# Kernel tuning notes

Hardware: AMD Instinct MI355X
Metric: run time of the kernel (lower is better)

Reference implementation:

```python
import jax, jax.numpy as jnp
import numpy as np

B, C, T = 128, 64, 128   # batch, num_channels (EEG electrodes), EEG_SEGMENT_LENGTH
HID = 128                # hidden_dim
E = HID // 2             # attention embed dim = 64
NH = 4                   # attention heads


def setup_inputs() -> dict:
    key = jax.random.key(0)
    ks = jax.random.split(key, 12)
    s = lambda k, shp, sc: jax.random.normal(k, shp, dtype=jnp.float32) * sc
    return {
        "eeg_data": jax.random.normal(ks[0], (B, C, T), dtype=jnp.float32),
        "gcn1_w": s(ks[1], (HID, T), 0.05),   # nn.Linear(T, HID): W [out,in]
        "gcn1_b": jnp.zeros((HID,), jnp.float32),
        "gcn2_w": s(ks[2], (E, HID), 0.05),
        "gcn2_b": jnp.zeros((E,), jnp.float32),
        "bn1_g": jnp.ones((C,), jnp.float32),
        "bn1_b": jnp.zeros((C,), jnp.float32),
        "bn2_g": jnp.ones((C,), jnp.float32),
        "bn2_b": jnp.zeros((C,), jnp.float32),
        "attn_in_w": s(ks[3], (3 * E, E), 0.08),   # packed q,k,v projection
        "attn_in_b": jnp.zeros((3 * E,), jnp.float32),
        "attn_out_w": s(ks[4], (E, E), 0.08),
        "attn_out_b": jnp.zeros((E,), jnp.float32),
    }


def _hilbert_phase(x):
    # torch.fft.fft -> zero bins [n//2:] (even n) -> *2 -> ifft -> angle
    n = x.shape[-1]
    half = n // 2 if n % 2 == 0 else (n + 1) // 2
    X = jnp.fft.fft(x, axis=-1)
    mask = (jnp.arange(n) < half).astype(jnp.float32) * 2.0
    analytic = jnp.fft.ifft(X * mask, axis=-1)
    return jnp.angle(analytic)


def _wpli(eeg):
    phase = _hilbert_phase(eeg)                         # [B,C,T]
    pd = phase[:, :, None, :] - phase[:, None, :, :]    # [B,C,C,T]
    pli = jnp.abs(jnp.mean(jnp.sign(jnp.sin(pd)), axis=-1))  # [B,C,C]
    eye = jnp.eye(pli.shape[-1], dtype=pli.dtype)
    return pli * (1.0 - eye)[None]


def _gcn(x, adj, w, b):
    # D^{-1/2} A D^{-1/2} via row/col scaling (equiv to diag_embed + bmm)
    deg = jnp.sum(adj, axis=2)                          # [B,C]
    dn = 1.0 / jnp.sqrt(deg + 1e-8)
    adj_n = adj * dn[:, :, None] * dn[:, None, :]
    support = jnp.einsum('bij,bjf->bif', adj_n, x)
    return support @ w.T + b


def _bn(x, g, b):
    # BatchNorm1d over channel dim C of [B,C,F]; batch stats over (B,F)
    m = jnp.mean(x, axis=(0, 2), keepdims=True)
    v = jnp.var(x, axis=(0, 2), keepdims=True)
    return (x - m) / jnp.sqrt(v + 1e-5) * g[None, :, None] + b[None, :, None]


def _mha(x, in_w, in_b, out_w, out_b):
    bsz, n, e = x.shape
    hd = e // NH
    qkv = x @ in_w.T + in_b                             # [B,N,3E]
    q, k, v = jnp.split(qkv, 3, axis=-1)
    sp = lambda t: t.reshape(bsz, n, NH, hd).transpose(0, 2, 1, 3)  # [B,H,N,hd]
    q, k, v = sp(q), sp(k), sp(v)
    scores = jnp.einsum('bhqd,bhkd->bhqk', q, k) / jnp.sqrt(jnp.float32(hd))
    attn = jax.nn.softmax(scores, axis=-1)
    o = jnp.einsum('bhqk,bhkd->bhqd', attn, v)
    o = o.transpose(0, 2, 1, 3).reshape(bsz, n, e)
    return o @ out_w.T + out_b


def reference(eeg_data, gcn1_w, gcn1_b, gcn2_w, gcn2_b, bn1_g, bn1_b,
              bn2_g, bn2_b, attn_in_w, attn_in_b, attn_out_w, attn_out_b):
    wpli = _wpli(eeg_data)                              # [B,C,C]
    x = jax.nn.relu(_bn(_gcn(eeg_data, wpli, gcn1_w, gcn1_b), bn1_g, bn1_b))
    x = jax.nn.relu(_bn(_gcn(x, wpli, gcn2_w, gcn2_b), bn2_g, bn2_b))
    x = _mha(x, attn_in_w, attn_in_b, attn_out_w, attn_out_b)
    features = jnp.mean(x, axis=1)                      # [B, E]
    return features, wpli
```

## Files before the change

### kernel.cpp

```cpp
#include <hip/hip_runtime.h>
#include <math.h>

#define NB 128
#define NC 64
#define NT 128
#define HIDN 128
#define NE 64
#define NHD 4
#define HD 16

__global__ void analytic_kernel(const float* __restrict__ eeg,
                                float* __restrict__ re, float* __restrict__ im) {
    int row = blockIdx.x;
    int t = threadIdx.x;
    __shared__ float xs[NT];
    __shared__ double cotv[64];
    xs[t] = eeg[row * NT + t];
    if (t < 64) {
        double d = (double)(2 * t + 1);
        double a = 3.14159265358979323846 * d / 128.0;
        cotv[t] = cos(a) / sin(a);
    }
    __syncthreads();
    double ar = 0.0, ai = 0.0;
    #pragma unroll
    for (int m = 0; m < 64; ++m) {
        int d = 2 * m + 1;
        int s = (t - d) & 127;
        double xv = (double)xs[s];
        ar += xv;
        ai += cotv[m] * xv;
    }
    double rr = (double)xs[t] + ar * (1.0 / 64.0);
    double ii = ai * (1.0 / 64.0);
    re[row * NT + t] = (float)rr;
    im[row * NT + t] = (float)ii;
}

__global__ void pli_kernel(const float* __restrict__ re, const float* __restrict__ im,
                           float* __restrict__ wpli, float* __restrict__ deg) {
    int b = blockIdx.x >> 4;
    int i0 = (blockIdx.x & 15) << 2;
    int tid = threadIdx.x;
    int w = tid >> 6;
    int j = tid & 63;
    __shared__ float4 sre4[64 * 32];
    __shared__ float4 sim4[64 * 32];
    __shared__ int pacc[4][4][64];
    const float* reb = re + b * (NC * NT);
    const float* imb = im + b * (NC * NT);
    for (int idx4 = tid; idx4 < 2048; idx4 += 256) {
        int c = idx4 >> 5, t4 = idx4 & 31;
        int slot = c * 32 + (t4 ^ (c & 31));
        sre4[slot] = ((const float4*)reb)[idx4];
        sim4[slot] = ((const float4*)imb)[idx4];
    }
    __syncthreads();
    int acc0 = 0, acc1 = 0, acc2 = 0, acc3 = 0;
    #pragma unroll
    for (int tt = 0; tt < 8; ++tt) {
        int t4 = w * 8 + tt;
        float4 rj = sre4[j * 32 + (t4 ^ (j & 31))];
        float4 ij = sim4[j * 32 + (t4 ^ (j & 31))];
        #pragma unroll
        for (int di = 0; di < 4; ++di) {
            int i = i0 + di;
            float4 ri = sre4[i * 32 + (t4 ^ (i & 31))];
            float4 ii = sim4[i * 32 + (t4 ^ (i & 31))];
            float c0 = ii.x * rj.x - ri.x * ij.x;
            float c1 = ii.y * rj.y - ri.y * ij.y;
            float c2 = ii.z * rj.z - ri.z * ij.z;
            float c3 = ii.w * rj.w - ri.w * ij.w;
            int d = ((c0 > 0.f) ? 1 : ((c0 < 0.f) ? -1 : 0))
                  + ((c1 > 0.f) ? 1 : ((c1 < 0.f) ? -1 : 0))
                  + ((c2 > 0.f) ? 1 : ((c2 < 0.f) ? -1 : 0))
                  + ((c3 > 0.f) ? 1 : ((c3 < 0.f) ? -1 : 0));
            if (di == 0) acc0 += d;
            else if (di == 1) acc1 += d;
            else if (di == 2) acc2 += d;
            else acc3 += d;
        }
    }
    pacc[w][0][j] = acc0; pacc[w][1][j] = acc1;
    pacc[w][2][j] = acc2; pacc[w][3][j] = acc3;
    __syncthreads();
    int di2 = tid >> 6, j2 = tid & 63;
    int a = pacc[0][di2][j2] + pacc[1][di2][j2] + pacc[2][di2][j2] + pacc[3][di2][j2];
    float p = fabsf((float)a * (1.f / (float)NT));
    int i = i0 + di2;
    if (j2 == i) p = 0.f;
    wpli[b * (NC * NC) + i * NC + j2] = p;
    float s = p;
    #pragma unroll
    for (int off = 32; off > 0; off >>= 1) s += __shfl_down(s, off);
    if (j2 == 0) deg[b * NC + i] = s;
}

template <int OUT, bool BN_IN>
__global__ __launch_bounds__(1024, 1) void gcn_fused(
        const float* __restrict__ adj, const float* __restrict__ deg,
        const float* __restrict__ x, const double* __restrict__ dpart_in,
        const float* __restrict__ g, const float* __restrict__ bb,
        const float* __restrict__ W, const float* __restrict__ bias,
        float* __restrict__ xout, double* __restrict__ dpart_out) {
    int b = blockIdx.x >> 1;
    int half = blockIdx.x & 1;
    int tid = threadIdx.x;
    __shared__ float dn_s[64];
    __shared__ float stat_s[64][2];
    __shared__ float arow[32][68];
    __shared__ float xs[64][128];
    __shared__ float sup[32][132];
    __shared__ float WsT[128][(OUT == 128) ? 132 : 68];
    __shared__ double dred[16][64][2];

    if (BN_IN) {
        int c = tid & 63, chunk = tid >> 6;
        double s = 0.0, s2 = 0.0;
        for (int bi = chunk * 8; bi < chunk * 8 + 8; ++bi) {
            s  += dpart_in[(bi * 64 + c) * 2];
            s2 += dpart_in[(bi * 64 + c) * 2 + 1];
        }
        dred[chunk][c][0] = s;
        dred[chunk][c][1] = s2;
    }
    if (tid < 64)
        dn_s[tid] = (float)(1.0 / sqrt((double)deg[b * 64 + tid] + 1e-8));
    __syncthreads();
    if (BN_IN && tid < 64) {
        double s = 0.0, s2 = 0.0;
        for (int ch = 0; ch < 16; ++ch) {
            s  += dred[ch][tid][0];
            s2 += dred[ch][tid][1];
        }
        double N = (double)(NB * HIDN);
        double m = s / N;
        double var = s2 / N - m * m;
        stat_s[tid][0] = (float)m;
        stat_s[tid][1] = (float)(1.0 / sqrt(var + 1e-5));
    }
    __syncthreads();
    if (tid < 512) {
        int il = tid >> 4, j4 = tid & 15;
        int i = half * 32 + il;
        float4 v = *(const float4*)&adj[b * 4096 + i * 64 + j4 * 4];
        float di = dn_s[i];
        v.x *= di * dn_s[j4 * 4 + 0];
        v.y *= di * dn_s[j4 * 4 + 1];
        v.z *= di * dn_s[j4 * 4 + 2];
        v.w *= di * dn_s[j4 * 4 + 3];
        *(float4*)&arow[il][j4 * 4] = v;
    }
    #pragma unroll
    for (int p = 0; p < 2; ++p) {
        int idx4 = tid + p * 1024;
        int r = idx4 >> 5, c4 = idx4 & 31;
        float4 v = ((const float4*)(x + b * 8192))[idx4];
        if (BN_IN) {
            float m = stat_s[r][0], rs = stat_s[r][1], gg = g[r], bv = bb[r];
            v.x = (v.x - m) * rs * gg + bv; v.x = v.x > 0.f ? v.x : 0.f;
            v.y = (v.y - m) * rs * gg + bv; v.y = v.y > 0.f ? v.y : 0.f;
            v.z = (v.z - m) * rs * gg + bv; v.z = v.z > 0.f ? v.z : 0.f;
            v.w = (v.w - m) * rs * gg + bv; v.w = v.w > 0.f ? v.w : 0.f;
        }
        *(float4*)&xs[r][c4 * 4] = v;
    }
    #pragma unroll
    for (int p = 0; p < OUT / 32; ++p) {
        int idx4 = tid + p * 1024;
        int o = idx4 & (OUT - 1);
        int k4 = idx4 / OUT;
        float4 w = *(const float4*)&W[o * 128 + k4 * 4];
        WsT[k4 * 4 + 0][o] = w.x;
        WsT[k4 * 4 + 1][o] = w.y;
        WsT[k4 * 4 + 2][o] = w.z;
        WsT[k4 * 4 + 3][o] = w.w;
    }
    __syncthreads();

    int il = tid >> 5;
    int i = half * 32 + il;
    {
        int f0 = (tid & 31) * 4;
        float a0 = 0.f, a1 = 0.f, a2 = 0.f, a3 = 0.f;
        #pragma unroll 8
        for (int j = 0; j < 64; ++j) {
            float a = arow[il][j];
            float4 xv = *(const float4*)&xs[j][f0];
            a0 += a * xv.x; a1 += a * xv.y; a2 += a * xv.z; a3 += a * xv.w;
        }
        *(float4*)&sup[il][f0] = make_float4(a0, a1, a2, a3);
    }
    __syncthreads();

    double ds = 0.0, ds2 = 0.0;
    if (OUT == 128) {
        int o0 = (tid & 31) * 4;
        float c[4] = {};
        #pragma unroll 8
        for (int k = 0; k < 128; ++k) {
            float s = sup[il][k];
            float4 w0 = *(const float4*)&WsT[k][o0];
            c[0] += s * w0.x; c[1] += s * w0.y; c[2] += s * w0.z; c[3] += s * w0.w;
        }
        float4 r0 = make_float4(c[0] + bias[o0], c[1] + bias[o0 + 1],
                                c[2] + bias[o0 + 2], c[3] + bias[o0 + 3]);
        *(float4*)&xout[b * 64 * 128 + i * 128 + o0] = r0;
        ds  = (double)r0.x + (double)r0.y + (double)r0.z + (double)r0.w;
        ds2 = (double)r0.x * r0.x + (double)r0.y * r0.y
            + (double)r0.z * r0.z + (double)r0.w * r0.w;
    } else {
        int o0 = (tid & 31) * 2;
        float c0 = 0.f, c1 = 0.f;
        #pragma unroll 8
        for (int k = 0; k < 128; ++k) {
            float s = sup[il][k];
            c0 += s * WsT[k][o0];
            c1 += s * WsT[k][o0 + 1];
        }
        c0 += bias[o0];
        c1 += bias[o0 + 1];
        *(float2*)&xout[b * 64 * 64 + i * 64 + o0] = make_float2(c0, c1);
        ds  = (double)c0 + (double)c1;
        ds2 = (double)c0 * c0 + (double)c1 * c1;
    }
    #pragma unroll
    for (int off = 16; off > 0; off >>= 1) {
        ds  += __shfl_down(ds, off, 32);
        ds2 += __shfl_down(ds2, off, 32);
    }
    if ((tid & 31) == 0) {
        dpart_out[(b * 64 + i) * 2]     = ds;
        dpart_out[(b * 64 + i) * 2 + 1] = ds2;
    }
}

__global__ __launch_bounds__(1024, 1) void attn_fused(
        const float* __restrict__ x2, const double* __restrict__ dpart2,
        const float* __restrict__ g, const float* __restrict__ bb,
        const float* __restrict__ Win, const float* __restrict__ bin,
        const float* __restrict__ Wout, const float* __restrict__ bout,
        float* __restrict__ feat) {
    int b = blockIdx.x;
    int tid = threadIdx.x;
    int lane = tid & 63, wv = tid >> 6;
    __shared__ float stat_s[64][2];
    __shared__ float xs[64][68];
    __shared__ float ws[192][64];
    __shared__ float kqkv[192][64];
    __shared__ float pm_s[4][256], ps_s[4][256];
    __shared__ float pool_s[64][17];
    __shared__ float mo[64];

    if (tid < 64) {
        double s = 0.0, s2 = 0.0;
        for (int bi = 0; bi < NB; ++bi) {
            s  += dpart2[(bi * 64 + tid) * 2];
            s2 += dpart2[(bi * 64 + tid) * 2 + 1];
        }
        double N = (double)(NB * NE);
        double m = s / N;
        double var = s2 / N - m * m;
        stat_s[tid][0] = (float)m;
        stat_s[tid][1] = (float)(1.0 / sqrt(var + 1e-5));
    }
    #pragma unroll
    for (int p = 0; p < 3; ++p) {
        int idx4 = tid + p * 1024;
        int o = idx4 >> 4, c4 = idx4 & 15;
        *(float4*)&ws[o][c4 * 4] = ((const float4*)(Win + o * 64))[c4];
    }
    __syncthreads();
    {
        int r = tid >> 4, c4 = tid & 15;
        float4 v = ((const float4*)(x2 + b * 4096))[tid];
        float m = stat_s[r][0], rs = stat_s[r][1], gg = g[r], bv = bb[r];
        v.x = (v.x - m) * rs * gg + bv; v.x = v.x > 0.f ? v.x : 0.f;
        v.y = (v.y - m) * rs * gg + bv; v.y = v.y > 0.f ? v.y : 0.f;
        v.z = (v.z - m) * rs * gg + bv; v.z = v.z > 0.f ? v.z : 0.f;
        v.w = (v.w - m) * rs * gg + bv; v.w = v.w > 0.f ? v.w : 0.f;
        *(float4*)&xs[r][c4 * 4] = v;
    }
    __syncthreads();

    float xr[64];
    #pragma unroll
    for (int d4 = 0; d4 < 16; ++d4) {
        float4 v = *(const float4*)&xs[lane][d4 * 4];
        xr[d4 * 4 + 0] = v.x; xr[d4 * 4 + 1] = v.y;
        xr[d4 * 4 + 2] = v.z; xr[d4 * 4 + 3] = v.w;
    }
    float acc[12];
    #pragma unroll
    for (int u = 0; u < 12; ++u) acc[u] = bin[wv + 16 * u];
    #pragma unroll
    for (int d4 = 0; d4 < 16; ++d4) {
        #pragma unroll
        for (int u = 0; u < 12; ++u) {
            float4 w = *(const float4*)&ws[wv + 16 * u][d4 * 4];
            acc[u] += xr[d4 * 4 + 0] * w.x + xr[d4 * 4 + 1] * w.y
                    + xr[d4 * 4 + 2] * w.z + xr[d4 * 4 + 3] * w.w;
        }
    }
    #pragma unroll
    for (int u = 0; u < 12; ++u) kqkv[wv + 16 * u][lane] = acc[u];
    __syncthreads();

    int h = wv >> 2, jc = wv & 3;
    int e0 = 16 * h, j0 = jc * 16, hn = h * 64 + lane;
    float q[16];
    #pragma unroll
    for (int d = 0; d < 16; ++d) q[d] = kqkv[e0 + d][lane];
    float sc[16];
    #pragma unroll
    for (int jj = 0; jj < 16; ++jj) sc[jj] = 0.f;
    #pragma unroll
    for (int d = 0; d < 16; ++d) {
        float qd = q[d];
        #pragma unroll
        for (int j4 = 0; j4 < 4; ++j4) {
            float4 kv = *(const float4*)&kqkv[64 + e0 + d][j0 + j4 * 4];
            sc[j4 * 4 + 0] += qd * kv.x;
            sc[j4 * 4 + 1] += qd * kv.y;
            sc[j4 * 4 + 2] += qd * kv.z;
            sc[j4 * 4 + 3] += qd * kv.w;
        }
    }
    float pmax = -1e30f;
    #pragma unroll
    for (int jj = 0; jj < 16; ++jj) { sc[jj] *= 0.25f; pmax = fmaxf(pmax, sc[jj]); }
    pm_s[jc][hn] = pmax;
    __syncthreads();
    float mx = fmaxf(fmaxf(pm_s[0][hn], pm_s[1][hn]),
                     fmaxf(pm_s[2][hn], pm_s[3][hn]));
    float psum = 0.f;
    #pragma unroll
    for (int jj = 0; jj < 16; ++jj) { sc[jj] = expf(sc[jj] - mx); psum += sc[jj]; }
    ps_s[jc][hn] = psum;
    float po[16];
    #pragma unroll
    for (int d = 0; d < 16; ++d) {
        float4 v0 = *(const float4*)&kqkv[128 + e0 + d][j0 + 0];
        float4 v1 = *(const float4*)&kqkv[128 + e0 + d][j0 + 4];
        float4 v2 = *(const float4*)&kqkv[128 + e0 + d][j0 + 8];
        float4 v3 = *(const float4*)&kqkv[128 + e0 + d][j0 + 12];
        po[d] = sc[0] * v0.x + sc[1] * v0.y + sc[2] * v0.z + sc[3] * v0.w
              + sc[4] * v1.x + sc[5] * v1.y + sc[6] * v1.z + sc[7] * v1.w
              + sc[8] * v2.x + sc[9] * v2.y + sc[10] * v2.z + sc[11] * v2.w
              + sc[12] * v3.x + sc[13] * v3.y + sc[14] * v3.z + sc[15] * v3.w;
    }
    __syncthreads();
    float inv = 1.f / (ps_s[0][hn] + ps_s[1][hn] + ps_s[2][hn] + ps_s[3][hn]);
    if (jc == 0) {
        #pragma unroll
        for (int d = 0; d < 16; ++d) kqkv[e0 + d][lane] = po[d];
    }
    __syncthreads();
    if (jc == 1) {
        #pragma unroll
        for (int d = 0; d < 16; ++d) kqkv[e0 + d][lane] += po[d];
    }
    __syncthreads();
    if (jc == 2) {
        #pragma unroll
        for (int d = 0; d < 16; ++d) kqkv[e0 + d][lane] += po[d];
    }
    __syncthreads();
    if (jc == 3) {
        #pragma unroll
        for (int d = 0; d < 16; ++d)
            kqkv[e0 + d][lane] = (kqkv[e0 + d][lane] + po[d]) * inv;
    }
    __syncthreads();
    {
        int e = tid >> 4, part = tid & 15;
        float4 v = *(const float4*)&kqkv[e][part * 4];
        pool_s[e][part] = v.x + v.y + v.z + v.w;
    }
    __syncthreads();
    if (tid < 64) {
        float s = 0.f;
        #pragma unroll
        for (int p = 0; p < 16; ++p) s += pool_s[tid][p];
        mo[tid] = s * (1.f / 64.f);
    }
    __syncthreads();
    if (tid < 64) {
        float a = bout[tid];
        const float4* wr = (const float4*)(Wout + tid * 64);
        #pragma unroll
        for (int d4 = 0; d4 < 16; ++d4) {
            float4 w = wr[d4];
            a += mo[d4 * 4 + 0] * w.x + mo[d4 * 4 + 1] * w.y
               + mo[d4 * 4 + 2] * w.z + mo[d4 * 4 + 3] * w.w;
        }
        feat[b * NE + tid] = a;
    }
}

extern "C" void kernel_launch(void* const* d_in, const int* in_sizes, int n_in,
                              void* d_out, int out_size, void* d_ws, size_t ws_size,
                              hipStream_t stream) {
    const float* eeg      = (const float*)d_in[0];
    const float* gcn1_w   = (const float*)d_in[1];
    const float* gcn1_b   = (const float*)d_in[2];
    const float* gcn2_w   = (const float*)d_in[3];
    const float* gcn2_b   = (const float*)d_in[4];
    const float* bn1_g    = (const float*)d_in[5];
    const float* bn1_b    = (const float*)d_in[6];
    const float* bn2_g    = (const float*)d_in[7];
    const float* bn2_b    = (const float*)d_in[8];
    const float* attn_in_w  = (const float*)d_in[9];
    const float* attn_in_b  = (const float*)d_in[10];
    const float* attn_out_w = (const float*)d_in[11];
    const float* attn_out_b = (const float*)d_in[12];

    float* out  = (float*)d_out;
    float* feat = out;
    float* wpli = out + NB * NE;

    float* ws = (float*)d_ws;
    float*  w_re   = ws;
    float*  w_im   = ws + 1048576;
    float*  w_x1   = ws + 2097152;
    float*  w_x2   = ws + 3145728;
    float*  w_deg  = ws + 3670016;
    double* dpart1 = (double*)(ws + 3678208);
    double* dpart2 = (double*)(ws + 3710976);

    analytic_kernel<<<NB * NC, NT, 0, stream>>>(eeg, w_re, w_im);
    pli_kernel<<<NB * NC / 4, 256, 0, stream>>>(w_re, w_im, wpli, w_deg);
    gcn_fused<HIDN, false><<<NB * 2, 1024, 0, stream>>>(
        wpli, w_deg, eeg, nullptr, nullptr, nullptr,
        gcn1_w, gcn1_b, w_x1, dpart1);
    gcn_fused<NE, true><<<NB * 2, 1024, 0, stream>>>(
        wpli, w_deg, w_x1, dpart1, bn1_g, bn1_b,
        gcn2_w, gcn2_b, w_x2, dpart2);
    attn_fused<<<NB, 1024, 0, stream>>>(w_x2, dpart2, bn2_g, bn2_b,
                                        attn_in_w, attn_in_b,
                                        attn_out_w, attn_out_b, feat);
}
```

Baseline: 103.2 us.

## Split attention kernel per head and move output projection to separate kernel

Replaces the one-block-per-batch 1024-thread attention kernel with 512 blocks of 256 threads, each handling one (batch, head) pair and loading only that head's slice of the QKV weights. The BN2 statistics reduction is spread across four waves instead of a single wave, and the pooled per-head outputs are written to workspace for a new small kernel that applies the output projection. The aim is more blocks and smaller shared-memory footprints so more CUs are busy, at the cost of an extra launch, a global round trip, and every block redundantly reducing the BN stats and normalizing the whole 64x64 input.

```diff
diff --git a/kernel.cpp b/kernel.cpp
--- a/kernel.cpp
+++ b/kernel.cpp
@@ -235,45 +235,45 @@
     }
 }
 
-__global__ __launch_bounds__(1024, 1) void attn_fused(
+__global__ __launch_bounds__(256) void attn_head(
         const float* __restrict__ x2, const double* __restrict__ dpart2,
         const float* __restrict__ g, const float* __restrict__ bb,
         const float* __restrict__ Win, const float* __restrict__ bin,
-        const float* __restrict__ Wout, const float* __restrict__ bout,
-        float* __restrict__ feat) {
-    int b = blockIdx.x;
+        float* __restrict__ w_mo) {
+    int b = blockIdx.x >> 2, h = blockIdx.x & 3;
     int tid = threadIdx.x;
     int lane = tid & 63, wv = tid >> 6;
+    __shared__ double dred[4][64][2];
     __shared__ float stat_s[64][2];
     __shared__ float xs[64][68];
-    __shared__ float ws[192][64];
-    __shared__ float kqkv[192][64];
-    __shared__ float pm_s[4][256], ps_s[4][256];
-    __shared__ float pool_s[64][17];
-    __shared__ float mo[64];
-
+    __shared__ float ws[48][64];
+    __shared__ float kqkv[48][64];
+    __shared__ float pm_s[4][64], ps_s[4][64];
+    __shared__ float pool_s[16][17];
+
+    {
+        double s = 0.0, s2 = 0.0;
+        for (int bi = wv * 32; bi < wv * 32 + 32; ++bi) {
+            s  += dpart2[(bi * 64 + lane) * 2];
+            s2 += dpart2[(bi * 64 + lane) * 2 + 1];
+        }
+        dred[wv][lane][0] = s;
+        dred[wv][lane][1] = s2;
+    }
+    __syncthreads();
     if (tid < 64) {
-        double s = 0.0, s2 = 0.0;
-        for (int bi = 0; bi < NB; ++bi) {
-            s  += dpart2[(bi * 64 + tid) * 2];
-            s2 += dpart2[(bi * 64 + tid) * 2 + 1];
-        }
+        double s  = dred[0][tid][0] + dred[1][tid][0] + dred[2][tid][0] + dred[3][tid][0];
+        double s2 = dred[0][tid][1] + dred[1][tid][1] + dred[2][tid][1] + dred[3][tid][1];
         double N = (double)(NB * NE);
         double m = s / N;
         double var = s2 / N - m * m;
         stat_s[tid][0] = (float)m;
         stat_s[tid][1] = (float)(1.0 / sqrt(var + 1e-5));
     }
-    #pragma unroll
-    for (int p = 0; p < 3; ++p) {
-        int idx4 = tid + p * 1024;
-        int o = idx4 >> 4, c4 = idx4 & 15;
-        *(float4*)&ws[o][c4 * 4] = ((const float4*)(Win + o * 64))[c4];
-    }
-    __syncthreads();
-    {
-        int r = tid >> 4, c4 = tid & 15;
-        float4 v = ((const float4*)(x2 + b * 4096))[tid];
+    __syncthreads();
+    for (int idx4 = tid; idx4 < 1024; idx4 += 256) {
+        int r = idx4 >> 4, c4 = idx4 & 15;
+        float4 v = ((const float4*)(x2 + b * 4096))[idx4];
         float m = stat_s[r][0], rs = stat_s[r][1], gg = g[r], bv = bb[r];
         v.x = (v.x - m) * rs * gg + bv; v.x = v.x > 0.f ? v.x : 0.f;
         v.y = (v.y - m) * rs * gg + bv; v.y = v.y > 0.f ? v.y : 0.f;
@@ -281,36 +281,36 @@
         v.w = (v.w - m) * rs * gg + bv; v.w = v.w > 0.f ? v.w : 0.f;
         *(float4*)&xs[r][c4 * 4] = v;
     }
-    __syncthreads();
-
-    float xr[64];
+    for (int idx4 = tid; idx4 < 768; idx4 += 256) {
+        int rl = idx4 >> 4, c4 = idx4 & 15;
+        int rg = ((rl >> 4) << 6) + (h << 4) + (rl & 15);
+        *(float4*)&ws[rl][c4 * 4] = ((const float4*)(Win + rg * 64))[c4];
+    }
+    __syncthreads();
+
+    float acc[12];
+    #pragma unroll
+    for (int u = 0; u < 12; ++u) {
+        int ol = wv + 4 * u;
+        acc[u] = bin[((ol >> 4) << 6) + (h << 4) + (ol & 15)];
+    }
     #pragma unroll
     for (int d4 = 0; d4 < 16; ++d4) {
-        float4 v = *(const float4*)&xs[lane][d4 * 4];
-        xr[d4 * 4 + 0] = v.x; xr[d4 * 4 + 1] = v.y;
-        xr[d4 * 4 + 2] = v.z; xr[d4 * 4 + 3] = v.w;
-    }
-    float acc[12];
-    #pragma unroll
-    for (int u = 0; u < 12; ++u) acc[u] = bin[wv + 16 * u];
-    #pragma unroll
-    for (int d4 = 0; d4 < 16; ++d4) {
+        float4 xv = *(const float4*)&xs[lane][d4 * 4];
         #pragma unroll
         for (int u = 0; u < 12; ++u) {
-            float4 w = *(const float4*)&ws[wv + 16 * u][d4 * 4];
-            acc[u] += xr[d4 * 4 + 0] * w.x + xr[d4 * 4 + 1] * w.y
-                    + xr[d4 * 4 + 2] * w.z + xr[d4 * 4 + 3] * w.w;
-        }
-    }
-    #pragma unroll
-    for (int u = 0; u < 12; ++u) kqkv[wv + 16 * u][lane] = acc[u];
-    __syncthreads();
-
-    int h = wv >> 2, jc = wv & 3;
-    int e0 = 16 * h, j0 = jc * 16, hn = h * 64 + lane;
+            float4 w = *(const float4*)&ws[wv + 4 * u][d4 * 4];
+            acc[u] += xv.x * w.x + xv.y * w.y + xv.z * w.z + xv.w * w.w;
+        }
+    }
+    #pragma unroll
+    for (int u = 0; u < 12; ++u) kqkv[wv + 4 * u][lane] = acc[u];
+    __syncthreads();
+
+    int j0 = wv * 16;
     float q[16];
     #pragma unroll
-    for (int d = 0; d < 16; ++d) q[d] = kqkv[e0 + d][lane];
+    for (int d = 0; d < 16; ++d) q[d] = kqkv[d][lane];
     float sc[16];
     #pragma unroll
     for (int jj = 0; jj < 16; ++jj) sc[jj] = 0.f;
@@ -319,7 +319,7 @@
         float qd = q[d];
         #pragma unroll
         for (int j4 = 0; j4 < 4; ++j4) {
-            float4 kv = *(const float4*)&kqkv[64 + e0 + d][j0 + j4 * 4];
+            float4 kv = *(const float4*)&kqkv[16 + d][j0 + j4 * 4];
             sc[j4 * 4 + 0] += qd * kv.x;
             sc[j4 * 4 + 1] += qd * kv.y;
             sc[j4 * 4 + 2] += qd * kv.z;
@@ -329,73 +329,81 @@
     float pmax = -1e30f;
     #pragma unroll
     for (int jj = 0; jj < 16; ++jj) { sc[jj] *= 0.25f; pmax = fmaxf(pmax, sc[jj]); }
-    pm_s[jc][hn] = pmax;
-    __syncthreads();
-    float mx = fmaxf(fmaxf(pm_s[0][hn], pm_s[1][hn]),
-                     fmaxf(pm_s[2][hn], pm_s[3][hn]));
+    pm_s[wv][lane] = pmax;
+    __syncthreads();
+    float mx = fmaxf(fmaxf(pm_s[0][lane], pm_s[1][lane]),
+                     fmaxf(pm_s[2][lane], pm_s[3][lane]));
     float psum = 0.f;
     #pragma unroll
     for (int jj = 0; jj < 16; ++jj) { sc[jj] = expf(sc[jj] - mx); psum += sc[jj]; }
-    ps_s[jc][hn] = psum;
+    ps_s[wv][lane] = psum;
     float po[16];
     #pragma unroll
     for (int d = 0; d < 16; ++d) {
-        float4 v0 = *(const float4*)&kqkv[128 + e0 + d][j0 + 0];
-        float4 v1 = *(const float4*)&kqkv[128 + e0 + d][j0 + 4];
-        float4 v2 = *(const float4*)&kqkv[128 + e0 + d][j0 + 8];
-        float4 v3 = *(const float4*)&kqkv[128 + e0 + d][j0 + 12];
+        float4 v0 = *(const float4*)&kqkv[32 + d][j0 + 0];
+        float4 v1 = *(const float4*)&kqkv[32 + d][j0 + 4];
+        float4 v2 = *(const float4*)&kqkv[32 + d][j0 + 8];
+        float4 v3 = *(const float4*)&kqkv[32 + d][j0 + 12];
         po[d] = sc[0] * v0.x + sc[1] * v0.y + sc[2] * v0.z + sc[3] * v0.w
               + sc[4] * v1.x + sc[5] * v1.y + sc[6] * v1.z + sc[7] * v1.w
               + sc[8] * v2.x + sc[9] * v2.y + sc[10] * v2.z + sc[11] * v2.w
               + sc[12] * v3.x + sc[13] * v3.y + sc[14] * v3.z + sc[15] * v3.w;
     }
     __syncthreads();
-    float inv = 1.f / (ps_s[0][hn] + ps_s[1][hn] + ps_s[2][hn] + ps_s[3][hn]);
-    if (jc == 0) {
-        #pragma unroll
-        for (int d = 0; d < 16; ++d) kqkv[e0 + d][lane] = po[d];
-    }
-    __syncthreads();
-    if (jc == 1) {
-        #pragma unroll
-        for (int d = 0; d < 16; ++d) kqkv[e0 + d][lane] += po[d];
-    }
-    __syncthreads();
-    if (jc == 2) {
-        #pragma unroll
-        for (int d = 0; d < 16; ++d) kqkv[e0 + d][lane] += po[d];
-    }
-    __syncthreads();
-    if (jc == 3) {
+    float inv = 1.f / (ps_s[0][lane] + ps_s[1][lane] + ps_s[2][lane] + ps_s[3][lane]);
+    if (wv == 0) {
+        #pragma unroll
+        for (int d = 0; d < 16; ++d) kqkv[d][lane] = po[d];
+    }
+    __syncthreads();
+    if (wv == 1) {
+        #pragma unroll
+        for (int d = 0; d < 16; ++d) kqkv[d][lane] += po[d];
+    }
+    __syncthreads();
+    if (wv == 2) {
+        #pragma unroll
+        for (int d = 0; d < 16; ++d) kqkv[d][lane] += po[d];
+    }
+    __syncthreads();
+    if (wv == 3) {
         #pragma unroll
         for (int d = 0; d < 16; ++d)
-            kqkv[e0 + d][lane] = (kqkv[e0 + d][lane] + po[d]) * inv;
+            kqkv[d][lane] = (kqkv[d][lane] + po[d]) * inv;
     }
     __syncthreads();
     {
-        int e = tid >> 4, part = tid & 15;
-        float4 v = *(const float4*)&kqkv[e][part * 4];
-        pool_s[e][part] = v.x + v.y + v.z + v.w;
-    }
-    __syncthreads();
-    if (tid < 64) {
+        int d = tid & 15, part = tid >> 4;
+        float4 v = *(const float4*)&kqkv[d][part * 4];
+        pool_s[d][part] = v.x + v.y + v.z + v.w;
+    }
+    __syncthreads();
+    if (tid < 16) {
         float s = 0.f;
         #pragma unroll
         for (int p = 0; p < 16; ++p) s += pool_s[tid][p];
-        mo[tid] = s * (1.f / 64.f);
-    }
-    __syncthreads();
-    if (tid < 64) {
-        float a = bout[tid];
-        const float4* wr = (const float4*)(Wout + tid * 64);
-        #pragma unroll
-        for (int d4 = 0; d4 < 16; ++d4) {
-            float4 w = wr[d4];
-            a += mo[d4 * 4 + 0] * w.x + mo[d4 * 4 + 1] * w.y
-               + mo[d4 * 4 + 2] * w.z + mo[d4 * 4 + 3] * w.w;
-        }
-        feat[b * NE + tid] = a;
-    }
+        w_mo[b * 64 + h * 16 + tid] = s * (1.f / 64.f);
+    }
+}
+
+__global__ void proj_kernel(const float* __restrict__ w_mo,
+                            const float* __restrict__ Wout,
+                            const float* __restrict__ bout,
+                            float* __restrict__ feat) {
+    int b = blockIdx.x;
+    int tid = threadIdx.x;
+    __shared__ float mos[64];
+    mos[tid] = w_mo[b * 64 + tid];
+    __syncthreads();
+    float acc = bout[tid];
+    const float4* wr = (const float4*)(Wout + tid * 64);
+    #pragma unroll
+    for (int d4 = 0; d4 < 16; ++d4) {
+        float4 w = wr[d4];
+        acc += mos[d4 * 4 + 0] * w.x + mos[d4 * 4 + 1] * w.y
+             + mos[d4 * 4 + 2] * w.z + mos[d4 * 4 + 3] * w.w;
+    }
+    feat[b * NE + tid] = acc;
 }
 
 extern "C" void kernel_launch(void* const* d_in, const int* in_sizes, int n_in,
@@ -425,8 +433,9 @@
     float*  w_x1   = ws + 2097152;
     float*  w_x2   = ws + 3145728;
     float*  w_deg  = ws + 3670016;
-    double* dpart1 = (double*)(ws + 3678208);
-    double* dpart2 = (double*)(ws + 3710976);
+    float*  w_mo   = ws + 3678208;
+    double* dpart1 = (double*)(ws + 3686400);
+    double* dpart2 = (double*)(ws + 3719168);
 
     analytic_kernel<<<NB * NC, NT, 0, stream>>>(eeg, w_re, w_im);
     pli_kernel<<<NB * NC / 4, 256, 0, stream>>>(w_re, w_im, wpli, w_deg);
@@ -436,7 +445,7 @@
     gcn_fused<NE, true><<<NB * 2, 1024, 0, stream>>>(
         wpli, w_deg, w_x1, dpart1, bn1_g, bn1_b,
         gcn2_w, gcn2_b, w_x2, dpart2);
-    attn_fused<<<NB, 1024, 0, stream>>>(w_x2, dpart2, bn2_g, bn2_b,
-                                        attn_in_w, attn_in_b,
-                                        attn_out_w, attn_out_b, feat);
-}
+    attn_head<<<NB * NHD, 256, 0, stream>>>(w_x2, dpart2, bn2_g, bn2_b,
+                                            attn_in_w, attn_in_b, w_mo);
+    proj_kernel<<<NB, NE, 0, stream>>>(w_mo, attn_out_w, attn_out_b, feat);
+}
```

Measured after the change: 98.73 us (median of 2 runs). 1.05x faster.
